# Kernel tuning notes

Measured on AMD Instinct MI355X. Metric: run time of the kernel, lower is better.

Reference implementation:

```python
import jax, jax.numpy as jnp
import numpy as np

N = 16384        # num particles (nodes)
E = 65536        # num edges (avg degree 4)
C = 32           # channels
IC = 64          # inter_channels
K = 16           # kernel taps = 4*4
EPS = 1e-5       # haiku BatchNorm default eps


def _conv_params(key, c_in, c_out):
    k1, k2 = jax.random.split(key)
    W = jax.random.normal(k1, (K, c_in, c_out), jnp.float32) / np.sqrt(K * c_in)
    P = jax.random.normal(k2, (3, K), jnp.float32)   # rel_pos -> kernel tap logits
    b = jnp.zeros((c_out,), jnp.float32)
    return W, P, b


def _bn_params(key, dim):
    k1, k2 = jax.random.split(key)
    scale = jnp.ones((dim,), jnp.float32)
    offset = jnp.zeros((dim,), jnp.float32)
    mean = 0.1 * jax.random.normal(k1, (dim,), jnp.float32)
    var = jax.random.uniform(k2, (dim,), jnp.float32, 0.5, 1.5)
    return scale, offset, mean, var


def setup_inputs() -> dict:
    key = jax.random.key(0)
    ks = jax.random.split(key, 16)
    d = {}
    d['x'] = jax.random.normal(ks[0], (N, C), jnp.float32)
    d['y'] = jax.random.normal(ks[1], (N, C), jnp.float32)
    d['senders'] = jax.random.randint(ks[2], (E,), 0, N)
    d['receivers'] = jax.random.randint(ks[3], (E,), 0, N)
    d['rel_pos'] = jax.random.normal(ks[4], (E, 3), jnp.float32)
    d['a'] = jax.random.uniform(ks[5], (E,), jnp.float32)
    dims = [(2 * C, IC), (IC, C), (C, IC), (IC, C)]
    for i, (ci, co) in enumerate(dims, start=1):
        W, P, b = _conv_params(ks[5 + i], ci, co)
        d[f'W{i}'], d[f'P{i}'], d[f'b{i}'] = W, P, b
        s, o, m, v = _bn_params(ks[9 + i], co)
        d[f's{i}'], d[f'o{i}'], d[f'm{i}'], d[f'v{i}'] = s, o, m, v
    return d


def _cconv(feat, senders, receivers, rel_pos, a, W, P, b):
    # Continuous conv: gather sender features, interpolate K kernel taps
    # from rel_pos, per-edge contraction, weight by a, scatter-add to receivers.
    fe = feat[senders]                                  # (E, Cin) gather
    w = jax.nn.softmax(rel_pos @ P, axis=-1)            # (E, K) tap weights
    fw = fe[:, None, :] * w[:, :, None]                 # (E, K, Cin)
    oe = jnp.einsum('eki,kio->eo', fw, W) * a[:, None]  # (E, Cout)
    return jax.ops.segment_sum(oe, receivers, num_segments=N) + b


def _bn(h, scale, offset, mean, var):
    # haiku BatchNorm, is_training=False (moving-average stats)
    return (h - mean) * jax.lax.rsqrt(var + EPS) * scale + offset


def reference(x, y, rel_pos, a,
              W1, P1, b1, s1, o1, m1, v1,
              W2, P2, b2, s2, o2, m2, v2,
              W3, P3, b3, s3, o3, m3, v3,
              W4, P4, b4, s4, o4, m4, v4,
              senders, receivers):
    xa = jnp.concatenate([x, y], axis=-1)               # (N, 2C)
    xl = _cconv(xa, senders, receivers, rel_pos, a, W1, P1, b1)
    xl = jax.nn.relu(_bn(xl, s1, o1, m1, v1))
    xl = _cconv(xl, senders, receivers, rel_pos, a, W2, P2, b2)
    xl = _bn(xl, s2, o2, m2, v2)
    wei1 = jax.nn.sigmoid(xl)
    xo = 2.0 * x * wei1 + 2.0 * y * (1.0 - wei1)        # first AFF fusion
    xl2 = _cconv(xo, senders, receivers, rel_pos, a, W3, P3, b3)
    xl2 = jax.nn.relu(_bn(xl2, s3, o3, m3, v3))
    xl2 = _cconv(xl2, senders, receivers, rel_pos, a, W4, P4, b4)
    xl2 = _bn(xl2, s4, o4, m4, v4)
    wei2 = jax.nn.sigmoid(xl2)
    return 2.0 * x * wei2 + 2.0 * y * (1.0 - wei2)      # second AFF fusion
```

## Files before the change

### kernel.cpp

```cpp
#include <hip/hip_runtime.h>
#include <hip/hip_bf16.h>

#define NN 16384
#define NE 65536

typedef __attribute__((ext_vector_type(8))) short short8;
typedef __attribute__((ext_vector_type(4))) float f32x4;

using bf16 = __hip_bfloat16;

__device__ __forceinline__ float b2f(bf16 v){ return __bfloat162float(v); }
__device__ __forceinline__ bf16 f2b(float v){ return __float2bfloat16(v); }

__global__ __launch_bounds__(256) void k_init(
    unsigned* __restrict__ curs,
    const float* __restrict__ rel, const float* __restrict__ a,
    const float* __restrict__ P1, const float* __restrict__ P2,
    const float* __restrict__ P3, const float* __restrict__ P4,
    float* __restrict__ g,
    const float* __restrict__ W1, const float* __restrict__ W2,
    const float* __restrict__ W3, const float* __restrict__ W4,
    bf16* __restrict__ Bp)
{
    int b = blockIdx.x;
    if(b < 64){
        curs[b*256 + threadIdx.x] = 0u;
        return;
    }
    if(b < 320){
        int e = (b-64)*256 + threadIdx.x;
        float r0 = rel[e*3+0], r1 = rel[e*3+1], r2 = rel[e*3+2];
        float av = a[e];
        const float* Ps[4] = {P1,P2,P3,P4};
        for(int c=0;c<4;c++){
            const float* P = Ps[c];
            float lg[16]; float mx = -1e30f;
            #pragma unroll
            for(int k=0;k<16;k++){
                float v = r0*P[k] + r1*P[16+k] + r2*P[32+k];
                lg[k] = v; mx = fmaxf(mx, v);
            }
            float ssum = 0.f;
            #pragma unroll
            for(int k=0;k<16;k++){ lg[k] = __expf(lg[k]-mx); ssum += lg[k]; }
            float inv = av/ssum;
            float* go = &g[((size_t)c*NE + e)*16];
            #pragma unroll
            for(int j=0;j<4;j++){
                ((float4*)go)[j] = make_float4(lg[j*4]*inv, lg[j*4+1]*inv,
                                               lg[j*4+2]*inv, lg[j*4+3]*inv);
            }
        }
        return;
    }
    int t = (b-320)*256 + threadIdx.x;
    const float* W; int Cout; int base; int tl;
    if(t < 8192)      { W=W1; Cout=64; base=0;     tl=t; }
    else if(t < 12288){ W=W2; Cout=32; base=8192;  tl=t-8192; }
    else if(t < 16384){ W=W3; Cout=64; base=12288; tl=t-12288; }
    else              { W=W4; Cout=32; base=16384; tl=t-16384; }
    int l  = tl & 63;
    int NCT = Cout >> 4;
    int ct = (tl >> 6) % NCT;
    int ks = (tl >> 6) / NCT;
    int col = ct*16 + (l & 15);
    int k0  = ks*32 + ((l >> 4) & 3)*8;
    short8 v;
    #pragma unroll
    for(int j=0;j<8;j++){
        bf16 h = f2b(W[(size_t)(k0+j)*Cout + col]);
        v[j] = (short)*(unsigned short*)&h;
    }
    ((short8*)Bp)[base + tl] = v;
}

__global__ __launch_bounds__(256) void k_countfill(const int* __restrict__ recv,
                                                   const int* __restrict__ send,
                                                   unsigned* __restrict__ curs,
                                                   unsigned* __restrict__ csr){
    int e = blockIdx.x*256 + threadIdx.x;
    if(e >= NE) return;
    int rv = recv[e];
    unsigned pos = atomicAdd(&curs[rv], 1u);
    if(pos < 32u) csr[(unsigned)rv*32u + pos] = ((unsigned)e << 14) | (unsigned)send[e];
}

template<int CIN, int NCT, int MODE, bool CONCAT, typename OT>
__global__ __launch_bounds__(256) void k_conv(
    const void* __restrict__ fAv, const float* __restrict__ fBv,
    const float* __restrict__ g,
    const unsigned* __restrict__ csr, const unsigned* __restrict__ curs,
    const bf16* __restrict__ Bp, const float* __restrict__ bias,
    const float* __restrict__ bns, const float* __restrict__ bno,
    const float* __restrict__ bnm, const float* __restrict__ bnv,
    const float* __restrict__ x, const float* __restrict__ y,
    OT* __restrict__ out)
{
    constexpr int KD   = CIN*16;
    constexpr int ROWB = KD*2;
    __shared__ __align__(16) char sT[16*ROWB];
    __shared__ float red[512];
    int wv = threadIdx.x >> 6, lane = threadIdx.x & 63;
    int nbase = blockIdx.x*16;

    const float* fAf = (const float*)fAv;
    const bf16*  fAb = (const bf16*)fAv;
    const int i     = (CIN==64) ? lane : (lane & 31);
    const int kbase = (CIN==64) ? 0 : ((lane >> 5) * 8);
    for(int t=0; t<4; t++){
        int nl   = wv*4 + t;
        int node = nbase + nl;
        unsigned cnt = curs[node]; if(cnt > 32u) cnt = 32u;
        constexpr int KPL = (CIN==64) ? 16 : 8;
        float acc[KPL];
        #pragma unroll
        for(int r=0;r<KPL;r++) acc[r] = 0.f;
        const unsigned* crow = csr + (unsigned)node*32u;
        for(unsigned j=0; j<cnt; j++){
            unsigned u = crow[j];
            int sid = (int)(u & 16383u);
            int eid = (int)(u >> 14);
            float fe;
            if(CONCAT){
                fe = (lane < 32) ? fAf[sid*32 + lane] : fBv[sid*32 + (lane-32)];
            } else {
                fe = b2f(fAb[sid*CIN + i]);
            }
            const float4* gp = (const float4*)&g[(size_t)eid*16 + kbase];
            if(CIN==64){
                float4 g0=gp[0], g1=gp[1], g2=gp[2], g3=gp[3];
                acc[0]  += g0.x*fe; acc[1]  += g0.y*fe; acc[2]  += g0.z*fe; acc[3]  += g0.w*fe;
                acc[4]  += g1.x*fe; acc[5]  += g1.y*fe; acc[6]  += g1.z*fe; acc[7]  += g1.w*fe;
                acc[8]  += g2.x*fe; acc[9]  += g2.y*fe; acc[10] += g2.z*fe; acc[11] += g2.w*fe;
                acc[12] += g3.x*fe; acc[13] += g3.y*fe; acc[14] += g3.z*fe; acc[15] += g3.w*fe;
            } else {
                float4 g0=gp[0], g1=gp[1];
                acc[0] += g0.x*fe; acc[1] += g0.y*fe; acc[2] += g0.z*fe; acc[3] += g0.w*fe;
                acc[4] += g1.x*fe; acc[5] += g1.y*fe; acc[6] += g1.z*fe; acc[7] += g1.w*fe;
            }
        }
        unsigned xo_ = (unsigned)((nl & 7) << 4);
        if(CIN==64){
            #pragma unroll
            for(int k=0;k<16;k++){
                unsigned byte = (unsigned)nl*ROWB + ((((unsigned)(k*64 + lane))*2u) ^ xo_);
                *(bf16*)(sT + byte) = f2b(acc[k]);
            }
        } else {
            #pragma unroll
            for(int r=0;r<8;r++){
                unsigned byte = (unsigned)nl*ROWB + ((((unsigned)((kbase+r)*32 + i))*2u) ^ xo_);
                *(bf16*)(sT + byte) = f2b(acc[r]);
            }
        }
    }
    __syncthreads();

    int r = lane & 15, h = lane >> 4;
    const short8* Bp8 = (const short8*)Bp;
    f32x4 acc4 = (f32x4){0.f,0.f,0.f,0.f};
    int c, ks0, ksn;
    if(NCT==4){ c = wv;      ks0 = 0;                ksn = KD/32; }
    else      { c = wv & 1;  ks0 = (wv>>1)*(KD/64);  ksn = KD/64; }
    unsigned xr = (unsigned)((r & 7) << 4);
    #pragma unroll 8
    for(int ks=ks0; ks<ks0+ksn; ks++){
        unsigned ab = (unsigned)r*ROWB + (((unsigned)(ks*64 + h*16)) ^ xr);
        short8 af  = *(const short8*)(sT + ab);
        short8 bfr = Bp8[(ks*NCT + c)*64 + lane];
        acc4 = __builtin_amdgcn_mfma_f32_16x16x32_bf16(af, bfr, acc4, 0, 0, 0);
    }
    if(NCT==2){
        if(wv >= 2){
            #pragma unroll
            for(int j=0;j<4;j++) red[c*256 + (h*4+j)*16 + r] = acc4[j];
        }
        __syncthreads();
        if(wv >= 2) return;
        #pragma unroll
        for(int j=0;j<4;j++) acc4[j] += red[c*256 + (h*4+j)*16 + r];
    }

    const int Cout = NCT*16;
    int col = c*16 + r;
    float inv = rsqrtf(bnv[col] + 1e-5f);
    float al  = bns[col] * inv;
    float be  = al*(bias[col] - bnm[col]) + bno[col];
    #pragma unroll
    for(int j=0;j<4;j++){
        int rr = nbase + h*4 + j;
        float v = al*acc4[j] + be;
        if(MODE==0){
            out[(size_t)rr*Cout + col] = (OT)fmaxf(v, 0.f);
        } else {
            float wei = 1.f/(1.f + __expf(-v));
            float xv = x[rr*32 + col];
            float yv = y[rr*32 + col];
            out[(size_t)rr*32 + col] = (OT)(2.f*xv*wei + 2.f*yv*(1.f - wei));
        }
    }
}

extern "C" void kernel_launch(void* const* d_in, const int* in_sizes, int n_in,
                              void* d_out, int out_size, void* d_ws, size_t ws_size,
                              hipStream_t stream){
    const float* x   = (const float*)d_in[0];
    const float* y   = (const float*)d_in[1];
    const int* send  = (const int*)d_in[2];
    const int* recv  = (const int*)d_in[3];
    const float* rel = (const float*)d_in[4];
    const float* a   = (const float*)d_in[5];
    const float *W[4], *P[4], *bb[4], *bs[4], *bo[4], *bm[4], *bv[4];
    for(int i=0;i<4;i++){
        int base = 6 + i*7;
        W[i]  = (const float*)d_in[base+0];
        P[i]  = (const float*)d_in[base+1];
        bb[i] = (const float*)d_in[base+2];
        bs[i] = (const float*)d_in[base+3];
        bo[i] = (const float*)d_in[base+4];
        bm[i] = (const float*)d_in[base+5];
        bv[i] = (const float*)d_in[base+6];
    }
    char* w = (char*)d_ws;
    float*    g    = (float*)(w);
    unsigned* curs = (unsigned*)(w + 16777216);
    unsigned* csr  = (unsigned*)(w + 16842752);
    bf16*     h1   = (bf16*)(w + 18939904);
    bf16*     xo   = (bf16*)(w + 21037056);
    bf16*     h3   = (bf16*)(w + 22085632);
    bf16*     Bp   = (bf16*)(w + 24182784);
    float*    outp = (float*)d_out;

    k_init     <<<400, 256, 0, stream>>>(curs, rel, a, P[0], P[1], P[2], P[3], g,
                                         W[0], W[1], W[2], W[3], Bp);
    k_countfill<<<NE/256, 256, 0, stream>>>(recv, send, curs, csr);

    (k_conv<64,4,0,true,bf16>)  <<<NN/16, 256, 0, stream>>>(x, y, g + (size_t)0*NE*16, csr, curs,
        Bp + (size_t)0*8,     bb[0], bs[0], bo[0], bm[0], bv[0], nullptr, nullptr, h1);
    (k_conv<64,2,1,false,bf16>) <<<NN/16, 256, 0, stream>>>(h1, nullptr, g + (size_t)1*NE*16, csr, curs,
        Bp + (size_t)8192*8,  bb[1], bs[1], bo[1], bm[1], bv[1], x, y, xo);
    (k_conv<32,4,0,false,bf16>) <<<NN/16, 256, 0, stream>>>(xo, nullptr, g + (size_t)2*NE*16, csr, curs,
        Bp + (size_t)12288*8, bb[2], bs[2], bo[2], bm[2], bv[2], nullptr, nullptr, h3);
    (k_conv<64,2,1,false,float>)<<<NN/16, 256, 0, stream>>>(h3, nullptr, g + (size_t)3*NE*16, csr, curs,
        Bp + (size_t)16384*8, bb[3], bs[3], bo[3], bm[3], bv[3], x, y, outp);
}
```

Baseline: 114.5 us.

## Assign one wave per node in conv kernels with 1024-thread blocks

Each conv block grows from 4 to 16 waves so each wave gathers one node's edges instead of four nodes serially. This exposes more memory-level parallelism in the latency-bound gather. The first eight CSR entries are prefetched as two vector loads and the gather loop is unrolled. The MFMA stage now runs on only NCT waves over the full K range, with no split-K reduction through shared memory, so most waves sit idle during the matmul and the NCT=2 layers lose some matmul parallelism.

Result: faster. 98.34 us (-14.1%).

```diff
diff --git a/kernel.cpp b/kernel.cpp
--- a/kernel.cpp
+++ b/kernel.cpp
@@ -86,7 +86,7 @@
 }
 
 template<int CIN, int NCT, int MODE, bool CONCAT, typename OT>
-__global__ __launch_bounds__(256) void k_conv(
+__global__ __launch_bounds__(1024, 4) void k_conv(
     const void* __restrict__ fAv, const float* __restrict__ fBv,
     const float* __restrict__ g,
     const unsigned* __restrict__ csr, const unsigned* __restrict__ curs,
@@ -99,86 +99,82 @@
     constexpr int KD   = CIN*16;
     constexpr int ROWB = KD*2;
     __shared__ __align__(16) char sT[16*ROWB];
-    __shared__ float red[512];
     int wv = threadIdx.x >> 6, lane = threadIdx.x & 63;
     int nbase = blockIdx.x*16;
+    int node  = nbase + wv;
+    int nl    = wv;
 
     const float* fAf = (const float*)fAv;
     const bf16*  fAb = (const bf16*)fAv;
     const int i     = (CIN==64) ? lane : (lane & 31);
     const int kbase = (CIN==64) ? 0 : ((lane >> 5) * 8);
-    for(int t=0; t<4; t++){
-        int nl   = wv*4 + t;
-        int node = nbase + nl;
-        unsigned cnt = curs[node]; if(cnt > 32u) cnt = 32u;
-        constexpr int KPL = (CIN==64) ? 16 : 8;
-        float acc[KPL];
+    unsigned cnt = curs[node]; if(cnt > 32u) cnt = 32u;
+    const unsigned* crow = csr + (unsigned)node*32u;
+    uint4 ca = ((const uint4*)crow)[0];
+    uint4 cb = ((const uint4*)crow)[1];
+    unsigned uu[8] = {ca.x, ca.y, ca.z, ca.w, cb.x, cb.y, cb.z, cb.w};
+
+    constexpr int KPL = (CIN==64) ? 16 : 8;
+    float acc[KPL];
+    #pragma unroll
+    for(int r=0;r<KPL;r++) acc[r] = 0.f;
+
+    auto edge = [&](unsigned u){
+        int sid = (int)(u & 16383u);
+        int eid = (int)(u >> 14);
+        float fe;
+        if(CONCAT){
+            fe = (lane < 32) ? fAf[sid*32 + lane] : fBv[sid*32 + (lane-32)];
+        } else {
+            fe = b2f(fAb[sid*CIN + i]);
+        }
+        const float4* gp = (const float4*)&g[(size_t)eid*16 + kbase];
+        if(CIN==64){
+            float4 g0=gp[0], g1=gp[1], g2=gp[2], g3=gp[3];
+            acc[0]  += g0.x*fe; acc[1]  += g0.y*fe; acc[2]  += g0.z*fe; acc[3]  += g0.w*fe;
+            acc[4]  += g1.x*fe; acc[5]  += g1.y*fe; acc[6]  += g1.z*fe; acc[7]  += g1.w*fe;
+            acc[8]  += g2.x*fe; acc[9]  += g2.y*fe; acc[10] += g2.z*fe; acc[11] += g2.w*fe;
+            acc[12] += g3.x*fe; acc[13] += g3.y*fe; acc[14] += g3.z*fe; acc[15] += g3.w*fe;
+        } else {
+            float4 g0=gp[0], g1=gp[1];
+            acc[0] += g0.x*fe; acc[1] += g0.y*fe; acc[2] += g0.z*fe; acc[3] += g0.w*fe;
+            acc[4] += g1.x*fe; acc[5] += g1.y*fe; acc[6] += g1.z*fe; acc[7] += g1.w*fe;
+        }
+    };
+    #pragma unroll
+    for(int j=0;j<8;j++){
+        if((unsigned)j < cnt) edge(uu[j]);
+    }
+    for(unsigned j=8; j<cnt; j++) edge(crow[j]);
+
+    unsigned xo_ = (unsigned)((nl & 7) << 4);
+    if(CIN==64){
         #pragma unroll
-        for(int r=0;r<KPL;r++) acc[r] = 0.f;
-        const unsigned* crow = csr + (unsigned)node*32u;
-        for(unsigned j=0; j<cnt; j++){
-            unsigned u = crow[j];
-            int sid = (int)(u & 16383u);
-            int eid = (int)(u >> 14);
-            float fe;
-            if(CONCAT){
-                fe = (lane < 32) ? fAf[sid*32 + lane] : fBv[sid*32 + (lane-32)];
-            } else {
-                fe = b2f(fAb[sid*CIN + i]);
-            }
-            const float4* gp = (const float4*)&g[(size_t)eid*16 + kbase];
-            if(CIN==64){
-                float4 g0=gp[0], g1=gp[1], g2=gp[2], g3=gp[3];
-                acc[0]  += g0.x*fe; acc[1]  += g0.y*fe; acc[2]  += g0.z*fe; acc[3]  += g0.w*fe;
-                acc[4]  += g1.x*fe; acc[5]  += g1.y*fe; acc[6]  += g1.z*fe; acc[7]  += g1.w*fe;
-                acc[8]  += g2.x*fe; acc[9]  += g2.y*fe; acc[10] += g2.z*fe; acc[11] += g2.w*fe;
-                acc[12] += g3.x*fe; acc[13] += g3.y*fe; acc[14] += g3.z*fe; acc[15] += g3.w*fe;
-            } else {
-                float4 g0=gp[0], g1=gp[1];
-                acc[0] += g0.x*fe; acc[1] += g0.y*fe; acc[2] += g0.z*fe; acc[3] += g0.w*fe;
-                acc[4] += g1.x*fe; acc[5] += g1.y*fe; acc[6] += g1.z*fe; acc[7] += g1.w*fe;
-            }
-        }
-        unsigned xo_ = (unsigned)((nl & 7) << 4);
-        if(CIN==64){
-            #pragma unroll
-            for(int k=0;k<16;k++){
-                unsigned byte = (unsigned)nl*ROWB + ((((unsigned)(k*64 + lane))*2u) ^ xo_);
-                *(bf16*)(sT + byte) = f2b(acc[k]);
-            }
-        } else {
-            #pragma unroll
-            for(int r=0;r<8;r++){
-                unsigned byte = (unsigned)nl*ROWB + ((((unsigned)((kbase+r)*32 + i))*2u) ^ xo_);
-                *(bf16*)(sT + byte) = f2b(acc[r]);
-            }
+        for(int k=0;k<16;k++){
+            unsigned byte = (unsigned)nl*ROWB + ((((unsigned)(k*64 + lane))*2u) ^ xo_);
+            *(bf16*)(sT + byte) = f2b(acc[k]);
+        }
+    } else {
+        #pragma unroll
+        for(int r=0;r<8;r++){
+            unsigned byte = (unsigned)nl*ROWB + ((((unsigned)((kbase+r)*32 + i))*2u) ^ xo_);
+            *(bf16*)(sT + byte) = f2b(acc[r]);
         }
     }
     __syncthreads();
 
+    if(wv >= NCT) return;
     int r = lane & 15, h = lane >> 4;
+    int c = wv;
     const short8* Bp8 = (const short8*)Bp;
     f32x4 acc4 = (f32x4){0.f,0.f,0.f,0.f};
-    int c, ks0, ksn;
-    if(NCT==4){ c = wv;      ks0 = 0;                ksn = KD/32; }
-    else      { c = wv & 1;  ks0 = (wv>>1)*(KD/64);  ksn = KD/64; }
     unsigned xr = (unsigned)((r & 7) << 4);
     #pragma unroll 8
-    for(int ks=ks0; ks<ks0+ksn; ks++){
+    for(int ks=0; ks<KD/32; ks++){
         unsigned ab = (unsigned)r*ROWB + (((unsigned)(ks*64 + h*16)) ^ xr);
         short8 af  = *(const short8*)(sT + ab);
         short8 bfr = Bp8[(ks*NCT + c)*64 + lane];
         acc4 = __builtin_amdgcn_mfma_f32_16x16x32_bf16(af, bfr, acc4, 0, 0, 0);
-    }
-    if(NCT==2){
-        if(wv >= 2){
-            #pragma unroll
-            for(int j=0;j<4;j++) red[c*256 + (h*4+j)*16 + r] = acc4[j];
-        }
-        __syncthreads();
-        if(wv >= 2) return;
-        #pragma unroll
-        for(int j=0;j<4;j++) acc4[j] += red[c*256 + (h*4+j)*16 + r];
     }
 
     const int Cout = NCT*16;
@@ -235,12 +231,12 @@
                                          W[0], W[1], W[2], W[3], Bp);
     k_countfill<<<NE/256, 256, 0, stream>>>(recv, send, curs, csr);
 
-    (k_conv<64,4,0,true,bf16>)  <<<NN/16, 256, 0, stream>>>(x, y, g + (size_t)0*NE*16, csr, curs,
+    (k_conv<64,4,0,true,bf16>)  <<<NN/16, 1024, 0, stream>>>(x, y, g + (size_t)0*NE*16, csr, curs,
         Bp + (size_t)0*8,     bb[0], bs[0], bo[0], bm[0], bv[0], nullptr, nullptr, h1);
-    (k_conv<64,2,1,false,bf16>) <<<NN/16, 256, 0, stream>>>(h1, nullptr, g + (size_t)1*NE*16, csr, curs,
+    (k_conv<64,2,1,false,bf16>) <<<NN/16, 1024, 0, stream>>>(h1, nullptr, g + (size_t)1*NE*16, csr, curs,
         Bp + (size_t)8192*8,  bb[1], bs[1], bo[1], bm[1], bv[1], x, y, xo);
-    (k_conv<32,4,0,false,bf16>) <<<NN/16, 256, 0, stream>>>(xo, nullptr, g + (size_t)2*NE*16, csr, curs,
+    (k_conv<32,4,0,false,bf16>) <<<NN/16, 1024, 0, stream>>>(xo, nullptr, g + (size_t)2*NE*16, csr, curs,
         Bp + (size_t)12288*8, bb[2], bs[2], bo[2], bm[2], bv[2], nullptr, nullptr, h3);
-    (k_conv<64,2,1,false,float>)<<<NN/16, 256, 0, stream>>>(h3, nullptr, g + (size_t)3*NE*16, csr, curs,
+    (k_conv<64,2,1,false,float>)<<<NN/16, 1024, 0, stream>>>(h3, nullptr, g + (size_t)3*NE*16, csr, curs,
         Bp + (size_t)16384*8, bb[3], bs[3], bo[3], bm[3], bv[3], x, y, outp);
 }
```
